# Kernel tuning notes

Hardware: AMD Instinct MI355X
Metric: run time of the kernel (lower is better)

## Reference

```python
import jax, jax.numpy as jnp
import numpy as np

N = 50000          # total atoms
M = 12             # max neighbours
N0 = 5000          # crystals (10 atoms each)
ORIG = 200
NBR = 64
AFL = 64           # atom_fea_len
NG = 3             # n_graph
HF = 128           # h_fea_len[0]
EPS = 1e-5


def _bn(x, g, b):
    # training-mode batchnorm1d: biased batch variance, eps=1e-5
    m = jnp.mean(x, axis=0)
    v = jnp.var(x, axis=0)
    return g * (x - m) * jax.lax.rsqrt(v + EPS) + b


def setup_inputs() -> dict:
    key = jax.random.key(0)
    ks = jax.random.split(key, 16)

    def lin(k, fi, fo):
        s = 1.0 / np.sqrt(fi)
        kw, kb = jax.random.split(k)
        return (jax.random.uniform(kw, (fi, fo), jnp.float32, -s, s),
                jax.random.uniform(kb, (fo,), jnp.float32, -s, s))

    emb_W, emb_b = lin(ks[0], ORIG, AFL)
    msg = [lin(jax.random.fold_in(ks[1], i), 2 * AFL + NBR, 2 * AFL) for i in range(NG)]
    msg_W = jnp.stack([w for w, _ in msg])            # (NG, 192, 128)
    msg_b = jnp.stack([b for _, b in msg])            # (NG, 128)
    bn2_g = jnp.ones((NG, 2 * AFL), jnp.float32)
    bn2_b = jnp.zeros((NG, 2 * AFL), jnp.float32)
    bn1_g = jnp.ones((NG, AFL), jnp.float32)
    bn1_b = jnp.zeros((NG, AFL), jnp.float32)
    fc1_W, fc1_b = lin(ks[2], 2 * AFL, HF)
    out_W, out_b = lin(ks[3], HF, 1)

    orig_atom_fea = jax.random.normal(ks[4], (N, ORIG), jnp.float32)
    nbr_fea = jax.random.normal(ks[5], (N, M, NBR), jnp.float32)
    nbr_fea_idx = jax.random.randint(ks[6], (N, M), 0, N, jnp.int64)
    segment_ids = (jnp.arange(N, dtype=jnp.int64) // (N // N0))  # sorted, 10 atoms/crystal

    return dict(orig_atom_fea=orig_atom_fea, nbr_fea=nbr_fea,
                nbr_fea_idx=nbr_fea_idx, segment_ids=segment_ids,
                emb_W=emb_W, emb_b=emb_b, msg_W=msg_W, msg_b=msg_b,
                bn2_g=bn2_g, bn2_b=bn2_b, bn1_g=bn1_g, bn1_b=bn1_b,
                fc1_W=fc1_W, fc1_b=fc1_b, out_W=out_W, out_b=out_b)


def _forward(orig_atom_fea, nbr_fea, nbr_fea_idx, segment_ids,
             emb_W, emb_b, msg_W, msg_b, bn2_g, bn2_b, bn1_g, bn1_b,
             fc1_W, fc1_b, out_W, out_b):
    atom = orig_atom_fea @ emb_W + emb_b                      # (N, AFL)

    for i in range(NG):
        nbr_atom = atom[nbr_fea_idx]                          # (N, M, AFL) gather
        self_atom = jnp.broadcast_to(atom[:, None, :], (N, M, AFL))
        total = jnp.concatenate([self_atom, nbr_atom, nbr_fea], axis=2)
        total = jnp.einsum('nmf,fo->nmo', total, msg_W[i]) + msg_b[i]
        total = _bn(total.reshape(-1, 2 * AFL), bn2_g[i], bn2_b[i]).reshape(N, M, 2 * AFL)
        nbr_filter, nbr_core = jnp.split(total, 2, axis=2)
        summed = jnp.sum(jax.nn.sigmoid(nbr_filter) * jax.nn.softplus(nbr_core), axis=1)
        summed = _bn(summed, bn1_g[i], bn1_b[i])
        atom = jax.nn.softplus(atom + summed)

    # pooling: per-crystal mean and unbiased std
    ones = jnp.ones((N,), atom.dtype)
    counts = jax.ops.segment_sum(ones, segment_ids, num_segments=N0)[:, None]
    mean = jax.ops.segment_sum(atom, segment_ids, num_segments=N0) / counts
    dev = atom - mean[segment_ids]
    ssq = jax.ops.segment_sum(dev * dev, segment_ids, num_segments=N0)
    std = jnp.sqrt(ssq / (counts - 1.0))                      # torch.std is unbiased
    crys = jnp.concatenate([mean, std], axis=1)               # (N0, 2*AFL)

    crys = jax.nn.softplus(crys)
    crys = jax.nn.softplus(crys @ fc1_W + fc1_b)
    return crys @ out_W + out_b                               # (N0, 1)


def reference(orig_atom_fea, nbr_fea, nbr_fea_idx, segment_ids,
              emb_W, emb_b, msg_W, msg_b, bn2_g, bn2_b, bn1_g, bn1_b,
              fc1_W, fc1_b, out_W, out_b):
    return _forward(orig_atom_fea, nbr_fea, nbr_fea_idx, segment_ids,
                    emb_W, emb_b, msg_W, msg_b, bn2_g, bn2_b, bn1_g, bn1_b,
                    fc1_W, fc1_b, out_W, out_b)
```

## Files before the change

### kernel.cpp

```cpp
#include <hip/hip_runtime.h>
#include <hip/hip_bf16.h>
#include <math.h>

#define N_ATOMS 50000
#define M_NBR   12
#define N0_CRYS 5000
#define ORIG_F  200
#define AFL     64
#define HF      128
#define EPS     1e-5f
#define NROWS   (N_ATOMS * M_NBR)
#define G1      1875
#define T1N     10
#define T2R     48
#define G2M     1250
#define T2N     10
#define EB_ROWS 16
#define GE      625

typedef float    f32x4  __attribute__((ext_vector_type(4)));
typedef unsigned u32x4  __attribute__((ext_vector_type(4)));
typedef short    bf16x8 __attribute__((ext_vector_type(8)));

__device__ __forceinline__ bf16x8 as_bf(u32x4 u) {
    union { u32x4 u; bf16x8 s; } x; x.u = u; return x.s;
}
#define MFMA_B(acc, a, b) \
    acc = __builtin_amdgcn_mfma_f32_16x16x32_bf16(as_bf(a), as_bf(b), acc, 0, 0, 0)

__device__ __forceinline__ float softplus_f(float x) {
    return fmaxf(x, 0.f) + __logf(1.f + __expf(-fabsf(x)));
}
__device__ __forceinline__ float sigmoid_f(float x) {
    return __builtin_amdgcn_rcpf(1.f + __expf(-x));
}
__device__ __forceinline__ float bf_lo(unsigned u) {
    union { unsigned i; float f; } x; x.i = u << 16; return x.f;
}
__device__ __forceinline__ float bf_hi(unsigned u) {
    union { unsigned i; float f; } x; x.i = u & 0xffff0000u; return x.f;
}
__device__ __forceinline__ ushort f2bf(float f) {
    union { float f; unsigned u; } x; x.f = f;
    unsigned r = x.u + 0x7fffu + ((x.u >> 16) & 1u);
    return (ushort)(r >> 16);
}
__device__ __forceinline__ float bf2f(ushort h) {
    union { unsigned i; float f; } x; x.i = ((unsigned)h) << 16; return x.f;
}

__global__ __launch_bounds__(256) void k_cvt_fea(const float* __restrict__ fea,
                                                 ushort* __restrict__ feaB)
{
    size_t i = ((size_t)blockIdx.x * 256 + threadIdx.x) * 8;
    float4 v0 = *(const float4*)(fea + i);
    float4 v1 = *(const float4*)(fea + i + 4);
    union { uint4 u; __hip_bfloat162 h[4]; } o;
    o.h[0] = __float22bfloat162_rn(make_float2(v0.x, v0.y));
    o.h[1] = __float22bfloat162_rn(make_float2(v0.z, v0.w));
    o.h[2] = __float22bfloat162_rn(make_float2(v1.x, v1.y));
    o.h[3] = __float22bfloat162_rn(make_float2(v1.z, v1.w));
    *(uint4*)(feaB + i) = o.u;
}

__global__ __launch_bounds__(256) void k_embed(const float* __restrict__ orig,
                                               const float* __restrict__ W,
                                               const float* __restrict__ b,
                                               float* __restrict__ atom)
{
    __shared__ float Wl[ORIG_F * AFL];
    __shared__ float rl[EB_ROWS * ORIG_F];
    for (int i = threadIdx.x * 4; i < ORIG_F * AFL; i += 256 * 4)
        *(float4*)&Wl[i] = *(const float4*)&W[i];
    const int c = threadIdx.x & 63;
    const int sub = threadIdx.x >> 6;
    const float bias = b[c];
    const int nchunks = N_ATOMS / EB_ROWS;
    for (int chunk = blockIdx.x; chunk < nchunks; chunk += GE) {
        size_t rbase = (size_t)chunk * EB_ROWS;
        __syncthreads();
        for (int i = threadIdx.x * 4; i < EB_ROWS * ORIG_F; i += 256 * 4)
            *(float4*)&rl[i] = *(const float4*)&orig[rbase * ORIG_F + i];
        __syncthreads();
        float a0 = bias, a1 = bias, a2 = bias, a3 = bias;
        const float* r0 = rl + (sub * 4 + 0) * ORIG_F;
        const float* r1 = rl + (sub * 4 + 1) * ORIG_F;
        const float* r2 = rl + (sub * 4 + 2) * ORIG_F;
        const float* r3 = rl + (sub * 4 + 3) * ORIG_F;
        #pragma unroll 2
        for (int f = 0; f < ORIG_F; f += 4) {
            float w0 = Wl[(f + 0) * AFL + c];
            float w1 = Wl[(f + 1) * AFL + c];
            float w2 = Wl[(f + 2) * AFL + c];
            float w3 = Wl[(f + 3) * AFL + c];
            float4 v0 = *(const float4*)(r0 + f);
            float4 v1 = *(const float4*)(r1 + f);
            float4 v2 = *(const float4*)(r2 + f);
            float4 v3 = *(const float4*)(r3 + f);
            a0 += v0.x * w0 + v0.y * w1 + v0.z * w2 + v0.w * w3;
            a1 += v1.x * w0 + v1.y * w1 + v1.z * w2 + v1.w * w3;
            a2 += v2.x * w0 + v2.y * w1 + v2.z * w2 + v2.w * w3;
            a3 += v3.x * w0 + v3.y * w1 + v3.z * w2 + v3.w * w3;
        }
        float* dst = atom + (rbase + sub * 4) * AFL + c;
        dst[0 * AFL] = a0; dst[1 * AFL] = a1; dst[2 * AFL] = a2; dst[3 * AFL] = a3;
    }
}

__global__ __launch_bounds__(256) void k_pproj(float* __restrict__ atom,
                                               const float* __restrict__ msgW,
                                               const float* __restrict__ msgB,
                                               float* __restrict__ Pself,
                                               __hip_bfloat16* __restrict__ PnbrB,
                                               const float* __restrict__ summed,
                                               const float* __restrict__ AB1,
                                               int layer)
{
    __shared__ float al[8][64];
    const int nbase = blockIdx.x * 8;
    for (int e = threadIdx.x; e < 512; e += 256) {
        int rr = e >> 6, c = e & 63;
        size_t gi = (size_t)(nbase + rr) * 64 + c;
        float a = atom[gi];
        if (layer > 0) {
            a = softplus_f(a + AB1[c] * summed[gi] + AB1[64 + c]);
            atom[gi] = a;
        }
        al[rr][c] = a;
    }
    int o = threadIdx.x & 127, half = threadIdx.x >> 7;
    const float* W = msgW + (size_t)layer * 192 * 128 + (size_t)half * 64 * 128;
    float wr[64];
    #pragma unroll
    for (int c = 0; c < 64; ++c) wr[c] = W[c * 128 + o];
    const float bias = (half == 0) ? msgB[layer * 128 + o] : 0.f;
    const int po = (o < 64) ? (2 * o) : (2 * (o - 64) + 1);
    __syncthreads();
    for (int a = 0; a < 8; ++a) {
        int n = nbase + a;
        const float4* ar = (const float4*)al[a];
        float a0 = bias, a1 = 0.f, a2 = 0.f, a3 = 0.f;
        #pragma unroll
        for (int cc = 0; cc < 16; ++cc) {
            float4 v = ar[cc];
            a0 += v.x * wr[4 * cc + 0];
            a1 += v.y * wr[4 * cc + 1];
            a2 += v.z * wr[4 * cc + 2];
            a3 += v.w * wr[4 * cc + 3];
        }
        float acc = (a0 + a1) + (a2 + a3);
        if (half == 0) Pself[(size_t)n * 128 + po] = acc;
        else           PnbrB[(size_t)n * 128 + po] = __float2bfloat16(acc);
    }
}

__global__ __launch_bounds__(256) void k_pass1s(const ushort* __restrict__ feaB,
                                                const int* __restrict__ nbr_idx,
                                                const float* __restrict__ Pself,
                                                const unsigned* __restrict__ PnbrI,
                                                const float* __restrict__ msgW,
                                                float* __restrict__ part, int layer)
{
    __shared__ ushort fl[2][32 * 64];
    const int tid = threadIdx.x;
    const int w = tid >> 6, lane = tid & 63, l15 = lane & 15, grp = lane >> 4;
    const float* We = msgW + (size_t)layer * 192 * 128 + (size_t)128 * 128;
    const int cf = w * 16 + l15;

    u32x4 bh[2][2];
    #pragma unroll
    for (int ct = 0; ct < 2; ++ct)
    #pragma unroll
    for (int ks = 0; ks < 2; ++ks) {
        int col = ct ? (64 + cf) : cf;
        unsigned ph[4];
        #pragma unroll
        for (int m = 0; m < 4; ++m) {
            float w0 = We[(ks * 32 + grp * 8 + 2 * m) * 128 + col];
            float w1 = We[(ks * 32 + grp * 8 + 2 * m + 1) * 128 + col];
            ph[m] = (unsigned)f2bf(w0) | ((unsigned)f2bf(w1) << 16);
        }
        bh[ct][ks] = (u32x4){ph[0], ph[1], ph[2], ph[3]};
    }

    const int srow = tid >> 3, sseg = tid & 7;
    const int soff = srow * 64 + ((sseg ^ (srow & 7)) << 3);

    float s0 = 0.f, s1 = 0.f, q0 = 0.f, q1 = 0.f;
    int tile = blockIdx.x;
    uint4 stg = *(const uint4*)(feaB + ((size_t)tile * 32 + srow) * 64 + sseg * 8);

    float2  psc[8];
    unsigned pnc[8];
    {
        #pragma unroll
        for (int i = 0; i < 8; ++i) {
            unsigned rg = (unsigned)tile * 32 + (i >> 2) * 16 + grp * 4 + (i & 3);
            unsigned idx = (unsigned)nbr_idx[rg];
            psc[i] = *(const float2*)(Pself + (size_t)((rg / 12u) * 128u + 2u * cf));
            pnc[i] = PnbrI[(idx << 6) + cf];
        }
    }

    int buf = 0;
    for (int t = 0; t < T1N; ++t, tile += G1) {
        *(uint4*)(fl[buf] + soff) = stg;
        __syncthreads();

        unsigned idxn[8]; float2 psn[8]; unsigned pnn[8];
        if (t < T1N - 1) {
            stg = *(const uint4*)(feaB + ((size_t)(tile + G1) * 32 + srow) * 64 + sseg * 8);
            #pragma unroll
            for (int i = 0; i < 8; ++i) {
                unsigned rg2 = (unsigned)(tile + G1) * 32 + (i >> 2) * 16 + grp * 4 + (i & 3);
                idxn[i] = (unsigned)nbr_idx[rg2];
                psn[i] = *(const float2*)(Pself + (size_t)((rg2 / 12u) * 128u + 2u * cf));
            }
        }

        f32x4 acc00 = {0.f,0.f,0.f,0.f}, acc01 = {0.f,0.f,0.f,0.f};
        f32x4 acc10 = {0.f,0.f,0.f,0.f}, acc11 = {0.f,0.f,0.f,0.f};
        {
            int o0 = l15 * 64 + ((grp ^ (l15 & 7)) << 3);
            int o1 = (16 + l15) * 64 + ((grp ^ (l15 & 7)) << 3);
            u32x4 a0 = *(const u32x4*)(fl[buf] + o0);
            u32x4 a1 = *(const u32x4*)(fl[buf] + o1);
            MFMA_B(acc00, a0, bh[0][0]);
            MFMA_B(acc01, a0, bh[1][0]);
            MFMA_B(acc10, a1, bh[0][0]);
            MFMA_B(acc11, a1, bh[1][0]);
        }
        {
            int o0 = l15 * 64 + (((4 + grp) ^ (l15 & 7)) << 3);
            int o1 = (16 + l15) * 64 + (((4 + grp) ^ (l15 & 7)) << 3);
            u32x4 a0 = *(const u32x4*)(fl[buf] + o0);
            u32x4 a1 = *(const u32x4*)(fl[buf] + o1);
            MFMA_B(acc00, a0, bh[0][1]);
            MFMA_B(acc01, a0, bh[1][1]);
            MFMA_B(acc10, a1, bh[0][1]);
            MFMA_B(acc11, a1, bh[1][1]);
        }

        if (t < T1N - 1) {
            #pragma unroll
            for (int i = 0; i < 8; ++i)
                pnn[i] = PnbrI[(idxn[i] << 6) + cf];
        }

        #pragma unroll
        for (int rt = 0; rt < 2; ++rt) {
            const f32x4& aA = rt ? acc10 : acc00;
            const f32x4& aB = rt ? acc11 : acc01;
            #pragma unroll
            for (int j = 0; j < 4; ++j) {
                int i = rt * 4 + j;
                float va = aA[j] + psc[i].x + bf_lo(pnc[i]);
                float vb = aB[j] + psc[i].y + bf_hi(pnc[i]);
                s0 += va; q0 += va * va; s1 += vb; q1 += vb * vb;
            }
        }
        if (t < T1N - 1) {
            #pragma unroll
            for (int i = 0; i < 8; ++i) { psc[i] = psn[i]; pnc[i] = pnn[i]; }
        }
        buf ^= 1;
    }

    s0 += __shfl_xor(s0, 16); s0 += __shfl_xor(s0, 32);
    s1 += __shfl_xor(s1, 16); s1 += __shfl_xor(s1, 32);
    q0 += __shfl_xor(q0, 16); q0 += __shfl_xor(q0, 32);
    q1 += __shfl_xor(q1, 16); q1 += __shfl_xor(q1, 32);
    if (lane < 16) {
        float* pb = part + (size_t)blockIdx.x * 256;
        pb[cf]            = s0;
        pb[64 + cf]       = s1;
        pb[128 + cf]      = q0;
        pb[192 + cf]      = q1;
    }
}

__global__ __launch_bounds__(256) void k_bn2_fin(const float* __restrict__ part,
                                                 const float* __restrict__ g,
                                                 const float* __restrict__ b,
                                                 float* __restrict__ AB,
                                                 int layer, int nb)
{
    int o = blockIdx.x;
    float s = 0.f, q = 0.f;
    for (int i = threadIdx.x; i < nb; i += 256) {
        s += part[i * 256 + o];
        q += part[i * 256 + 128 + o];
    }
    __shared__ float rs[256], rq[256];
    rs[threadIdx.x] = s; rq[threadIdx.x] = q;
    __syncthreads();
    for (int st = 128; st > 0; st >>= 1) {
        if (threadIdx.x < st) {
            rs[threadIdx.x] += rs[threadIdx.x + st];
            rq[threadIdx.x] += rq[threadIdx.x + st];
        }
        __syncthreads();
    }
    if (threadIdx.x == 0) {
        const float inv_n = 1.0f / (float)NROWS;
        float m = rs[0] * inv_n;
        float v = rq[0] * inv_n - m * m;
        float A = g[layer * 128 + o] * rsqrtf(v + EPS);
        AB[o] = A;
        AB[128 + o] = b[layer * 128 + o] - A * m;
    }
}

__global__ __launch_bounds__(256) void k_pass2m(const ushort* __restrict__ feaB,
                                                const int* __restrict__ nbr_idx,
                                                const float* __restrict__ Pself,
                                                const unsigned* __restrict__ PnbrI,
                                                const float* __restrict__ msgW,
                                                const float* __restrict__ AB,
                                                float* __restrict__ summed,
                                                float* __restrict__ part, int layer)
{
    __shared__ ushort fl[2][T2R * 64];
    const int tid = threadIdx.x;
    const int w = tid >> 6, lane = tid & 63, l15 = lane & 15, grp = lane >> 4;
    const float* We = msgW + (size_t)layer * 192 * 128 + (size_t)128 * 128;
    const int cf = w * 16 + l15;

    u32x4 bh[2][2], bl[2][2];
    #pragma unroll
    for (int ct = 0; ct < 2; ++ct)
    #pragma unroll
    for (int ks = 0; ks < 2; ++ks) {
        int col = ct ? (64 + cf) : cf;
        unsigned ph[4], pl[4];
        #pragma unroll
        for (int m = 0; m < 4; ++m) {
            float w0 = We[(ks * 32 + grp * 8 + 2 * m) * 128 + col];
            float w1 = We[(ks * 32 + grp * 8 + 2 * m + 1) * 128 + col];
            ushort h0 = f2bf(w0), h1 = f2bf(w1);
            ushort g0 = f2bf(w0 - bf2f(h0)), g1 = f2bf(w1 - bf2f(h1));
            ph[m] = (unsigned)h0 | ((unsigned)h1 << 16);
            pl[m] = (unsigned)g0 | ((unsigned)g1 << 16);
        }
        bh[ct][ks] = (u32x4){ph[0], ph[1], ph[2], ph[3]};
        bl[ct][ks] = (u32x4){pl[0], pl[1], pl[2], pl[3]};
    }

    const float Af = AB[cf],      Bf = AB[128 + cf];
    const float Ac = AB[64 + cf], Bc = AB[192 + cf];

    const int ar0 = (4 * grp) / 12;
    const int ar1 = (16 + 4 * grp) / 12;
    const int ar2 = (32 + 4 * grp) / 12;

    const int row0 = tid >> 3, seg0 = tid & 7;
    const int soff0 = row0 * 64 + ((seg0 ^ (row0 & 7)) << 3);
    const int row1 = row0 + 32, seg1 = seg0;
    const int soff1 = row1 * 64 + ((seg1 ^ (row1 & 7)) << 3);

    float sstat = 0.f, qstat = 0.f;
    int tile = blockIdx.x;

    uint4 stgA = *(const uint4*)(feaB + ((size_t)tile * T2R + row0) * 64 + seg0 * 8);
    uint4 stgB;
    if (tid < 128)
        stgB = *(const uint4*)(feaB + ((size_t)tile * T2R + row1) * 64 + seg1 * 8);

    unsigned idxc[12];
    float psF[3], psC[3];
    {
        #pragma unroll
        for (int rt = 0; rt < 3; ++rt)
            #pragma unroll
            for (int j = 0; j < 4; ++j)
                idxc[rt * 4 + j] = (unsigned)nbr_idx[(size_t)tile * T2R + 16 * rt + 4 * grp + j];
        unsigned n0 = (unsigned)tile * 4;
        float2 p0 = *(const float2*)(Pself + (size_t)((n0 + ar0) * 128u + 2u * cf));
        float2 p1 = *(const float2*)(Pself + (size_t)((n0 + ar1) * 128u + 2u * cf));
        float2 p2 = *(const float2*)(Pself + (size_t)((n0 + ar2) * 128u + 2u * cf));
        psF[0] = p0.x; psC[0] = p0.y;
        psF[1] = p1.x; psC[1] = p1.y;
        psF[2] = p2.x; psC[2] = p2.y;
    }

    int buf = 0;
    for (int t = 0; t < T2N; ++t, tile += G2M) {
        *(uint4*)(fl[buf] + soff0) = stgA;
        if (tid < 128) *(uint4*)(fl[buf] + soff1) = stgB;
        __syncthreads();

        unsigned pnv[12];
        #pragma unroll
        for (int i = 0; i < 12; ++i)
            pnv[i] = PnbrI[(idxc[i] << 6) + cf];

        unsigned idxn[12]; float psFn[3], psCn[3];
        if (t < T2N - 1) {
            int tn = tile + G2M;
            stgA = *(const uint4*)(feaB + ((size_t)tn * T2R + row0) * 64 + seg0 * 8);
            if (tid < 128)
                stgB = *(const uint4*)(feaB + ((size_t)tn * T2R + row1) * 64 + seg1 * 8);
            #pragma unroll
            for (int rt = 0; rt < 3; ++rt)
                #pragma unroll
                for (int j = 0; j < 4; ++j)
                    idxn[rt * 4 + j] = (unsigned)nbr_idx[(size_t)tn * T2R + 16 * rt + 4 * grp + j];
            unsigned n0 = (unsigned)tn * 4;
            float2 p0 = *(const float2*)(Pself + (size_t)((n0 + ar0) * 128u + 2u * cf));
            float2 p1 = *(const float2*)(Pself + (size_t)((n0 + ar1) * 128u + 2u * cf));
            float2 p2 = *(const float2*)(Pself + (size_t)((n0 + ar2) * 128u + 2u * cf));
            psFn[0] = p0.x; psCn[0] = p0.y;
            psFn[1] = p1.x; psCn[1] = p1.y;
            psFn[2] = p2.x; psCn[2] = p2.y;
        }

        f32x4 aF0 = {0.f,0.f,0.f,0.f}, aC0 = {0.f,0.f,0.f,0.f};
        f32x4 aF1 = {0.f,0.f,0.f,0.f}, aC1 = {0.f,0.f,0.f,0.f};
        f32x4 aF2 = {0.f,0.f,0.f,0.f}, aC2 = {0.f,0.f,0.f,0.f};
        #pragma unroll
        for (int rt = 0; rt < 3; ++rt) {
            f32x4& aF = rt == 0 ? aF0 : rt == 1 ? aF1 : aF2;
            f32x4& aC = rt == 0 ? aC0 : rt == 1 ? aC1 : aC2;
            int R = rt * 16 + l15;
            int o0 = R * 64 + ((grp ^ (l15 & 7)) << 3);
            int o1 = R * 64 + (((4 + grp) ^ (l15 & 7)) << 3);
            u32x4 a0 = *(const u32x4*)(fl[buf] + o0);
            u32x4 a1 = *(const u32x4*)(fl[buf] + o1);
            MFMA_B(aF, a0, bh[0][0]); MFMA_B(aF, a0, bl[0][0]);
            MFMA_B(aC, a0, bh[1][0]); MFMA_B(aC, a0, bl[1][0]);
            MFMA_B(aF, a1, bh[0][1]); MFMA_B(aF, a1, bl[0][1]);
            MFMA_B(aC, a1, bh[1][1]); MFMA_B(aC, a1, bl[1][1]);
        }

        float prt[3];
        #pragma unroll
        for (int rt = 0; rt < 3; ++rt) {
            const f32x4& aF = rt == 0 ? aF0 : rt == 1 ? aF1 : aF2;
            const f32x4& aC = rt == 0 ? aC0 : rt == 1 ? aC1 : aC2;
            const float psf = psF[rt], psc_ = psC[rt];
            float acc = 0.f;
            #pragma unroll
            for (int j = 0; j < 4; ++j) {
                unsigned pn = pnv[rt * 4 + j];
                float va = aF[j] + psf  + bf_lo(pn);
                float vb = aC[j] + psc_ + bf_hi(pn);
                acc += sigmoid_f(Af * va + Bf) * softplus_f(Ac * vb + Bc);
            }
            prt[rt] = acc;
        }

        float c0 = (grp < 3) ? prt[0] : 0.f;
        float c1 = (grp == 3 ? prt[0] : 0.f) + (grp < 2 ? prt[1] : 0.f);
        float c2 = (grp >= 2 ? prt[1] : 0.f) + (grp == 0 ? prt[2] : 0.f);
        float c3 = (grp >= 1) ? prt[2] : 0.f;
        c0 += __shfl_xor(c0, 16); c0 += __shfl_xor(c0, 32);
        c1 += __shfl_xor(c1, 16); c1 += __shfl_xor(c1, 32);
        c2 += __shfl_xor(c2, 16); c2 += __shfl_xor(c2, 32);
        c3 += __shfl_xor(c3, 16); c3 += __shfl_xor(c3, 32);
        float v = (grp & 2) ? ((grp & 1) ? c3 : c2) : ((grp & 1) ? c1 : c0);
        summed[(size_t)((unsigned)(tile * 4 + grp) * 64u + cf)] = v;
        sstat += v; qstat += v * v;

        if (t < T2N - 1) {
            #pragma unroll
            for (int i = 0; i < 12; ++i) idxc[i] = idxn[i];
            #pragma unroll
            for (int rt = 0; rt < 3; ++rt) { psF[rt] = psFn[rt]; psC[rt] = psCn[rt]; }
        }
        buf ^= 1;
    }

    sstat += __shfl_xor(sstat, 16); sstat += __shfl_xor(sstat, 32);
    qstat += __shfl_xor(qstat, 16); qstat += __shfl_xor(qstat, 32);
    if (lane < 16) {
        float* pb = part + (size_t)blockIdx.x * 128;
        pb[cf] = sstat;
        pb[64 + cf] = qstat;
    }
}

__global__ __launch_bounds__(256) void k_bn1_fin(const float* __restrict__ part,
                                                 const float* __restrict__ g,
                                                 const float* __restrict__ b,
                                                 float* __restrict__ AB1,
                                                 int layer, int nb)
{
    int c = blockIdx.x;
    float s = 0.f, q = 0.f;
    for (int i = threadIdx.x; i < nb; i += 256) {
        s += part[i * 128 + c];
        q += part[i * 128 + 64 + c];
    }
    __shared__ float rs[256], rq[256];
    rs[threadIdx.x] = s; rq[threadIdx.x] = q;
    __syncthreads();
    for (int st = 128; st > 0; st >>= 1) {
        if (threadIdx.x < st) {
            rs[threadIdx.x] += rs[threadIdx.x + st];
            rq[threadIdx.x] += rq[threadIdx.x + st];
        }
        __syncthreads();
    }
    if (threadIdx.x == 0) {
        const float inv_n = 1.0f / (float)N_ATOMS;
        float m = rs[0] * inv_n;
        float v = rq[0] * inv_n - m * m;
        float A = g[layer * 64 + c] * rsqrtf(v + EPS);
        AB1[c] = A;
        AB1[64 + c] = b[layer * 64 + c] - A * m;
    }
}

__global__ __launch_bounds__(128) void k_pool_head(const float* __restrict__ atom,
                                                   const float* __restrict__ summed,
                                                   const float* __restrict__ AB1,
                                                   const float* __restrict__ fc1W,
                                                   const float* __restrict__ fc1b,
                                                   const float* __restrict__ outW,
                                                   const float* __restrict__ outb,
                                                   float* __restrict__ out)
{
    __shared__ float cry[128];
    __shared__ float red[128];
    for (int ci = blockIdx.x; ci < N0_CRYS; ci += gridDim.x) {
        if (threadIdx.x < 64) {
            int c = threadIdx.x;
            float A1 = AB1[c], B1 = AB1[64 + c];
            const float* ap = atom + (size_t)ci * 10 * 64 + c;
            const float* sp = summed + (size_t)ci * 10 * 64 + c;
            float v[10]; float s = 0.f;
            #pragma unroll
            for (int k = 0; k < 10; ++k) {
                v[k] = softplus_f(ap[k * 64] + A1 * sp[k * 64] + B1);
                s += v[k];
            }
            float mn = s * 0.1f;
            float ss = 0.f;
            #pragma unroll
            for (int k = 0; k < 10; ++k) { float d = v[k] - mn; ss += d * d; }
            cry[c]      = softplus_f(mn);
            cry[64 + c] = softplus_f(sqrtf(ss * (1.f / 9.f)));
        }
        __syncthreads();
        int o = threadIdx.x;
        float a0 = fc1b[o], a1 = 0.f;
        #pragma unroll 8
        for (int f = 0; f < 128; f += 2) {
            a0 += cry[f]     * fc1W[f * 128 + o];
            a1 += cry[f + 1] * fc1W[(f + 1) * 128 + o];
        }
        red[o] = softplus_f(a0 + a1) * outW[o];
        __syncthreads();
        for (int st = 64; st > 0; st >>= 1) {
            if (threadIdx.x < st) red[threadIdx.x] += red[threadIdx.x + st];
            __syncthreads();
        }
        if (threadIdx.x == 0) out[ci] = red[0] + outb[0];
        __syncthreads();
    }
}

extern "C" void kernel_launch(void* const* d_in, const int* in_sizes, int n_in,
                              void* d_out, int out_size, void* d_ws, size_t ws_size,
                              hipStream_t stream)
{
    const float* orig    = (const float*)d_in[0];
    const float* nbr_fea = (const float*)d_in[1];
    const int*   nbr_idx = (const int*)d_in[2];
    const float* embW = (const float*)d_in[4];
    const float* embB = (const float*)d_in[5];
    const float* msgW = (const float*)d_in[6];
    const float* msgB = (const float*)d_in[7];
    const float* bn2g = (const float*)d_in[8];
    const float* bn2b = (const float*)d_in[9];
    const float* bn1g = (const float*)d_in[10];
    const float* bn1b = (const float*)d_in[11];
    const float* fc1W = (const float*)d_in[12];
    const float* fc1b = (const float*)d_in[13];
    const float* outW = (const float*)d_in[14];
    const float* outb = (const float*)d_in[15];
    float* out = (float*)d_out;

    char* w = (char*)d_ws;
    auto take = [&](size_t n) { void* p = (void*)w; w += (n + 255) & ~(size_t)255; return p; };
    float*  atom   = (float*)take((size_t)N_ATOMS * 64 * 4);
    float*  Pself  = (float*)take((size_t)N_ATOMS * 128 * 4);
    __hip_bfloat16* PnbrB = (__hip_bfloat16*)take((size_t)N_ATOMS * 128 * 2);
    float*  summed = (float*)take((size_t)N_ATOMS * 64 * 4);
    float*  part   = (float*)take((size_t)4096 * 256 * 4);
    float*  AB     = (float*)take(256 * 4);
    float*  AB1    = (float*)take(128 * 4);
    ushort* feaB   = (ushort*)take((size_t)NROWS * 64 * 2);
    (void)ws_size;

    k_cvt_fea<<<dim3(18750), dim3(256), 0, stream>>>(nbr_fea, feaB);
    k_embed<<<dim3(GE), dim3(256), 0, stream>>>(orig, embW, embB, atom);

    for (int i = 0; i < 3; ++i) {
        k_pproj<<<dim3(6250), dim3(256), 0, stream>>>(atom, msgW, msgB, Pself, PnbrB,
                                                      summed, AB1, i);
        k_pass1s<<<dim3(G1), dim3(256), 0, stream>>>(feaB, nbr_idx, Pself,
                                                     (const unsigned*)PnbrB, msgW, part, i);
        k_bn2_fin<<<dim3(128), dim3(256), 0, stream>>>(part, bn2g, bn2b, AB, i, G1);
        k_pass2m<<<dim3(G2M), dim3(256), 0, stream>>>(feaB, nbr_idx, Pself,
                                                      (const unsigned*)PnbrB, msgW, AB,
                                                      summed, part, i);
        k_bn1_fin<<<dim3(64), dim3(256), 0, stream>>>(part, bn1g, bn1b, AB1, i, G2M);
    }

    k_pool_head<<<dim3(1024), dim3(128), 0, stream>>>(atom, summed, AB1,
                                                      fc1W, fc1b, outW, outb, out);
}
```

Baseline: 553.4 us.

## Move per-layer atom projection to bf16x3 MFMA and merge prep kernels

Rewrites the per-layer self/neighbour projection as a matrix-core kernel: each block takes 32 atoms, splits activations and weights into bf16 hi/lo parts (three MFMAs per product to keep near-fp32 accuracy), and stages atoms in swizzled LDS. This replaces the scalar FMA loop that reloaded 64 weights per thread for every 8 atoms. It also merges the fp32-to-bf16 feature conversion and the embedding kernel into one launch. The workspace buffers are padded for the last partial block. The cost is three times the MFMA work, weight splitting repeated in every block, and the bf16x3 rounding behaviour.

```diff
diff --git a/kernel.cpp b/kernel.cpp
--- a/kernel.cpp
+++ b/kernel.cpp
@@ -17,6 +17,8 @@
 #define T2N     10
 #define EB_ROWS 16
 #define GE      625
+#define GCVT    18750
+#define GPJ     1563
 
 typedef float    f32x4  __attribute__((ext_vector_type(4)));
 typedef unsigned u32x4  __attribute__((ext_vector_type(4)));
@@ -49,34 +51,35 @@
     union { unsigned i; float f; } x; x.i = ((unsigned)h) << 16; return x.f;
 }
 
-__global__ __launch_bounds__(256) void k_cvt_fea(const float* __restrict__ fea,
-                                                 ushort* __restrict__ feaB)
-{
-    size_t i = ((size_t)blockIdx.x * 256 + threadIdx.x) * 8;
-    float4 v0 = *(const float4*)(fea + i);
-    float4 v1 = *(const float4*)(fea + i + 4);
-    union { uint4 u; __hip_bfloat162 h[4]; } o;
-    o.h[0] = __float22bfloat162_rn(make_float2(v0.x, v0.y));
-    o.h[1] = __float22bfloat162_rn(make_float2(v0.z, v0.w));
-    o.h[2] = __float22bfloat162_rn(make_float2(v1.x, v1.y));
-    o.h[3] = __float22bfloat162_rn(make_float2(v1.z, v1.w));
-    *(uint4*)(feaB + i) = o.u;
-}
-
-__global__ __launch_bounds__(256) void k_embed(const float* __restrict__ orig,
-                                               const float* __restrict__ W,
-                                               const float* __restrict__ b,
-                                               float* __restrict__ atom)
+__global__ __launch_bounds__(256) void k_prep(const float* __restrict__ fea,
+                                              ushort* __restrict__ feaB,
+                                              const float* __restrict__ orig,
+                                              const float* __restrict__ W,
+                                              const float* __restrict__ b,
+                                              float* __restrict__ atom)
 {
     __shared__ float Wl[ORIG_F * AFL];
     __shared__ float rl[EB_ROWS * ORIG_F];
+    if (blockIdx.x < GCVT) {
+        size_t i = ((size_t)blockIdx.x * 256 + threadIdx.x) * 8;
+        float4 v0 = *(const float4*)(fea + i);
+        float4 v1 = *(const float4*)(fea + i + 4);
+        union { uint4 u; __hip_bfloat162 h[4]; } o;
+        o.h[0] = __float22bfloat162_rn(make_float2(v0.x, v0.y));
+        o.h[1] = __float22bfloat162_rn(make_float2(v0.z, v0.w));
+        o.h[2] = __float22bfloat162_rn(make_float2(v1.x, v1.y));
+        o.h[3] = __float22bfloat162_rn(make_float2(v1.z, v1.w));
+        *(uint4*)(feaB + i) = o.u;
+        return;
+    }
+    const int bid = blockIdx.x - GCVT;
     for (int i = threadIdx.x * 4; i < ORIG_F * AFL; i += 256 * 4)
         *(float4*)&Wl[i] = *(const float4*)&W[i];
     const int c = threadIdx.x & 63;
     const int sub = threadIdx.x >> 6;
     const float bias = b[c];
     const int nchunks = N_ATOMS / EB_ROWS;
-    for (int chunk = blockIdx.x; chunk < nchunks; chunk += GE) {
+    for (int chunk = bid; chunk < nchunks; chunk += GE) {
         size_t rbase = (size_t)chunk * EB_ROWS;
         __syncthreads();
         for (int i = threadIdx.x * 4; i < EB_ROWS * ORIG_F; i += 256 * 4)
@@ -107,50 +110,120 @@
     }
 }
 
-__global__ __launch_bounds__(256) void k_pproj(float* __restrict__ atom,
-                                               const float* __restrict__ msgW,
-                                               const float* __restrict__ msgB,
-                                               float* __restrict__ Pself,
-                                               __hip_bfloat16* __restrict__ PnbrB,
-                                               const float* __restrict__ summed,
-                                               const float* __restrict__ AB1,
-                                               int layer)
-{
-    __shared__ float al[8][64];
-    const int nbase = blockIdx.x * 8;
-    for (int e = threadIdx.x; e < 512; e += 256) {
-        int rr = e >> 6, c = e & 63;
-        size_t gi = (size_t)(nbase + rr) * 64 + c;
-        float a = atom[gi];
+__global__ __launch_bounds__(256) void k_pprojm(float* __restrict__ atom,
+                                                const float* __restrict__ msgW,
+                                                const float* __restrict__ msgB,
+                                                float* __restrict__ Pself,
+                                                __hip_bfloat16* __restrict__ PnbrB,
+                                                const float* __restrict__ summed,
+                                                const float* __restrict__ AB1,
+                                                int layer)
+{
+    __shared__ ushort ah[32 * 64], al[32 * 64];
+    const int tid = threadIdx.x;
+    const int w = tid >> 6, lane = tid & 63, l15 = lane & 15, grp = lane >> 4;
+    const int cf = w * 16 + l15;
+    const int n0 = blockIdx.x * 32;
+
+    {
+        const int row = tid >> 3, seg = tid & 7;
+        int n = n0 + row;
+        int nr = n < N_ATOMS ? n : N_ATOMS - 1;
+        size_t gi = (size_t)nr * 64 + seg * 8;
+        float4 v0 = *(const float4*)(atom + gi);
+        float4 v1 = *(const float4*)(atom + gi + 4);
+        float a[8] = {v0.x, v0.y, v0.z, v0.w, v1.x, v1.y, v1.z, v1.w};
         if (layer > 0) {
-            a = softplus_f(a + AB1[c] * summed[gi] + AB1[64 + c]);
-            atom[gi] = a;
-        }
-        al[rr][c] = a;
-    }
-    int o = threadIdx.x & 127, half = threadIdx.x >> 7;
-    const float* W = msgW + (size_t)layer * 192 * 128 + (size_t)half * 64 * 128;
-    float wr[64];
-    #pragma unroll
-    for (int c = 0; c < 64; ++c) wr[c] = W[c * 128 + o];
-    const float bias = (half == 0) ? msgB[layer * 128 + o] : 0.f;
-    const int po = (o < 64) ? (2 * o) : (2 * (o - 64) + 1);
+            float4 s0 = *(const float4*)(summed + gi);
+            float4 s1 = *(const float4*)(summed + gi + 4);
+            float sv[8] = {s0.x, s0.y, s0.z, s0.w, s1.x, s1.y, s1.z, s1.w};
+            #pragma unroll
+            for (int k = 0; k < 8; ++k) {
+                int cc = seg * 8 + k;
+                a[k] = softplus_f(a[k] + AB1[cc] * sv[k] + AB1[64 + cc]);
+            }
+            if (n < N_ATOMS) {
+                float4 o0 = {a[0], a[1], a[2], a[3]}, o1 = {a[4], a[5], a[6], a[7]};
+                *(float4*)(atom + gi)     = o0;
+                *(float4*)(atom + gi + 4) = o1;
+            }
+        }
+        ushort hb[8], lb[8];
+        #pragma unroll
+        for (int k = 0; k < 8; ++k) {
+            hb[k] = f2bf(a[k]);
+            lb[k] = f2bf(a[k] - bf2f(hb[k]));
+        }
+        int soff = row * 64 + ((seg ^ (row & 7)) << 3);
+        *(uint4*)(ah + soff) = *(uint4*)hb;
+        *(uint4*)(al + soff) = *(uint4*)lb;
+    }
+
+    const float* W = msgW + (size_t)layer * 192 * 128;
+    u32x4 wh[2][2][2], wl[2][2][2];
+    #pragma unroll
+    for (int mat = 0; mat < 2; ++mat)
+    #pragma unroll
+    for (int ct = 0; ct < 2; ++ct)
+    #pragma unroll
+    for (int ks = 0; ks < 2; ++ks) {
+        int col = ct ? (64 + cf) : cf;
+        const float* Wm = W + (size_t)mat * 64 * 128;
+        unsigned ph[4], pl[4];
+        #pragma unroll
+        for (int m = 0; m < 4; ++m) {
+            float w0 = Wm[(ks * 32 + grp * 8 + 2 * m) * 128 + col];
+            float w1 = Wm[(ks * 32 + grp * 8 + 2 * m + 1) * 128 + col];
+            ushort h0 = f2bf(w0), h1 = f2bf(w1);
+            ushort g0 = f2bf(w0 - bf2f(h0)), g1 = f2bf(w1 - bf2f(h1));
+            ph[m] = (unsigned)h0 | ((unsigned)h1 << 16);
+            pl[m] = (unsigned)g0 | ((unsigned)g1 << 16);
+        }
+        wh[mat][ct][ks] = (u32x4){ph[0], ph[1], ph[2], ph[3]};
+        wl[mat][ct][ks] = (u32x4){pl[0], pl[1], pl[2], pl[3]};
+    }
+    const float biasF = msgB[layer * 128 + cf];
+    const float biasC = msgB[layer * 128 + 64 + cf];
     __syncthreads();
-    for (int a = 0; a < 8; ++a) {
-        int n = nbase + a;
-        const float4* ar = (const float4*)al[a];
-        float a0 = bias, a1 = 0.f, a2 = 0.f, a3 = 0.f;
-        #pragma unroll
-        for (int cc = 0; cc < 16; ++cc) {
-            float4 v = ar[cc];
-            a0 += v.x * wr[4 * cc + 0];
-            a1 += v.y * wr[4 * cc + 1];
-            a2 += v.z * wr[4 * cc + 2];
-            a3 += v.w * wr[4 * cc + 3];
-        }
-        float acc = (a0 + a1) + (a2 + a3);
-        if (half == 0) Pself[(size_t)n * 128 + po] = acc;
-        else           PnbrB[(size_t)n * 128 + po] = __float2bfloat16(acc);
+
+    f32x4 acc[2][2][2];
+    #pragma unroll
+    for (int mat = 0; mat < 2; ++mat)
+    #pragma unroll
+    for (int rt = 0; rt < 2; ++rt)
+    #pragma unroll
+    for (int ct = 0; ct < 2; ++ct)
+        acc[mat][rt][ct] = (f32x4){0.f, 0.f, 0.f, 0.f};
+
+    #pragma unroll
+    for (int rt = 0; rt < 2; ++rt)
+    #pragma unroll
+    for (int ks = 0; ks < 2; ++ks) {
+        int off = (rt * 16 + l15) * 64 + (((ks * 4 + grp) ^ (l15 & 7)) << 3);
+        u32x4 aH = *(const u32x4*)(ah + off);
+        u32x4 aL = *(const u32x4*)(al + off);
+        #pragma unroll
+        for (int mat = 0; mat < 2; ++mat)
+        #pragma unroll
+        for (int ct = 0; ct < 2; ++ct) {
+            MFMA_B(acc[mat][rt][ct], aH, wh[mat][ct][ks]);
+            MFMA_B(acc[mat][rt][ct], aH, wl[mat][ct][ks]);
+            MFMA_B(acc[mat][rt][ct], aL, wh[mat][ct][ks]);
+        }
+    }
+
+    #pragma unroll
+    for (int rt = 0; rt < 2; ++rt)
+    #pragma unroll
+    for (int j = 0; j < 4; ++j) {
+        int n = n0 + rt * 16 + grp * 4 + j;
+        if (n < N_ATOMS) {
+            float2 ps = {acc[0][rt][0][j] + biasF, acc[0][rt][1][j] + biasC};
+            *(float2*)(Pself + (size_t)n * 128 + 2 * cf) = ps;
+            unsigned pk = (unsigned)f2bf(acc[1][rt][0][j]) |
+                          ((unsigned)f2bf(acc[1][rt][1][j]) << 16);
+            *(unsigned*)((ushort*)PnbrB + (size_t)n * 128 + 2 * cf) = pk;
+        }
     }
 }
 
@@ -583,21 +656,20 @@
 
     char* w = (char*)d_ws;
     auto take = [&](size_t n) { void* p = (void*)w; w += (n + 255) & ~(size_t)255; return p; };
-    float*  atom   = (float*)take((size_t)N_ATOMS * 64 * 4);
+    float*  atom   = (float*)take((size_t)(N_ATOMS + 32) * 64 * 4);
     float*  Pself  = (float*)take((size_t)N_ATOMS * 128 * 4);
     __hip_bfloat16* PnbrB = (__hip_bfloat16*)take((size_t)N_ATOMS * 128 * 2);
-    float*  summed = (float*)take((size_t)N_ATOMS * 64 * 4);
+    float*  summed = (float*)take((size_t)(N_ATOMS + 32) * 64 * 4);
     float*  part   = (float*)take((size_t)4096 * 256 * 4);
     float*  AB     = (float*)take(256 * 4);
     float*  AB1    = (float*)take(128 * 4);
     ushort* feaB   = (ushort*)take((size_t)NROWS * 64 * 2);
     (void)ws_size;
 
-    k_cvt_fea<<<dim3(18750), dim3(256), 0, stream>>>(nbr_fea, feaB);
-    k_embed<<<dim3(GE), dim3(256), 0, stream>>>(orig, embW, embB, atom);
+    k_prep<<<dim3(GCVT + GE), dim3(256), 0, stream>>>(nbr_fea, feaB, orig, embW, embB, atom);
 
     for (int i = 0; i < 3; ++i) {
-        k_pproj<<<dim3(6250), dim3(256), 0, stream>>>(atom, msgW, msgB, Pself, PnbrB,
+        k_pprojm<<<dim3(GPJ), dim3(256), 0, stream>>>(atom, msgW, msgB, Pself, PnbrB,
                                                       summed, AB1, i);
         k_pass1s<<<dim3(G1), dim3(256), 0, stream>>>(feaB, nbr_idx, Pself,
                                                      (const unsigned*)PnbrB, msgW, part, i);
```

Result: faster. 501.6 us (-9.4%).
